# Kernel optimization log

Measured on AMD Instinct MI355X. Metric: run time of the kernel, lower is better.

Reference implementation:

```python
import jax, jax.numpy as jnp
import numpy as np

DIM = 1024
HEADS = 16
HEAD_DIM = DIM // HEADS


def setup_inputs() -> dict:
    key = jax.random.key(0)
    ks = jax.random.split(key, 10)
    B, N, M = 4, 2048, 2048
    s = 1.0 / np.sqrt(DIM)
    return {
        "x": jax.random.normal(ks[0], (B, N, DIM), jnp.float32),
        "context": jax.random.normal(ks[1], (B, M, DIM), jnp.float32),
        "Wq": jax.random.normal(ks[2], (DIM, DIM), jnp.float32) * s,
        "bq": jnp.zeros((DIM,), jnp.float32),
        "Wk": jax.random.normal(ks[3], (DIM, DIM), jnp.float32) * s,
        "bk": jnp.zeros((DIM,), jnp.float32),
        "Wv": jax.random.normal(ks[4], (DIM, DIM), jnp.float32) * s,
        "bv": jnp.zeros((DIM,), jnp.float32),
        "Wo": jax.random.normal(ks[5], (DIM, DIM), jnp.float32) * s,
        "bo": jnp.zeros((DIM,), jnp.float32),
    }


def reference(x, context, Wq, bq, Wk, bk, Wv, bv, Wo, bo):
    B, N, C = x.shape
    M = context.shape[1]
    scale = HEAD_DIM ** (-0.5)
    # projections + split heads: [B, H, L, D]
    q = (x @ Wq.T + bq).reshape(B, N, HEADS, HEAD_DIM).transpose(0, 2, 1, 3)
    k = (context @ Wk.T + bk).reshape(B, M, HEADS, HEAD_DIM).transpose(0, 2, 1, 3)
    v = (context @ Wv.T + bv).reshape(B, M, HEADS, HEAD_DIM).transpose(0, 2, 1, 3)
    attn = jax.nn.softmax(jnp.einsum('bhnd,bhmd->bhnm', q, k) * scale, axis=-1)
    out = jnp.einsum('bhnm,bhmd->bhnd', attn, v)  # [B, H, N, D]
    out = out.transpose(0, 2, 1, 3).reshape(B, N, C)
    return out @ Wo.T + bo
```

## Files before the change

### kernel.cpp

```cpp
#include <hip/hip_runtime.h>
#include <hip/hip_bf16.h>
#include <stdint.h>


#define HEADS 16
#define HD 64
#define NSEQ 2048
#define DIMSZ 1024

typedef __bf16 bf16x8_t __attribute__((ext_vector_type(8)));
typedef float f32x4_t __attribute__((ext_vector_type(4)));
typedef short s16x4 __attribute__((ext_vector_type(4)));
typedef unsigned short u16;
typedef unsigned int u32;

__device__ __forceinline__ u16 f2bf(float f) {
    union { float f; u32 i; } x; x.f = f;
    u32 r = x.i + 0x7FFF + ((x.i >> 16) & 1);
    return (u16)(r >> 16);
}
__device__ __forceinline__ u32 pk2(float a, float b) {
    __hip_bfloat162 h = __float22bfloat162_rn(float2{a, b});
    union { __hip_bfloat162 h2; u32 u; } c; c.h2 = h; return c.u;
}

#if defined(__has_builtin)
#if __has_builtin(__builtin_amdgcn_exp2f)
#define EXP2(x) __builtin_amdgcn_exp2f(x)
#endif
#endif
#ifndef EXP2
#define EXP2(x) exp2f(x)
#endif

__device__ __forceinline__ void pl32swap(u32& a, u32& b) {
    asm("v_permlane32_swap_b32 %0, %1" : "+v"(a), "+v"(b));
}
__device__ __forceinline__ void pl16swap(u32& a, u32& b) {
    asm("v_permlane16_swap_b32 %0, %1" : "+v"(a), "+v"(b));
}

#define GLDS(g, l) __builtin_amdgcn_global_load_lds( \
    (const __attribute__((address_space(1))) void*)(g), \
    (__attribute__((address_space(3))) void*)(l), 16, 0, 0)

__global__ __launch_bounds__(256)
void cvt_all(const float* __restrict__ x, const float* __restrict__ ctx,
             const float* __restrict__ wq, const float* __restrict__ wk,
             const float* __restrict__ wv, const float* __restrict__ wo,
             u16* __restrict__ xb, u16* __restrict__ ctxb,
             u16* __restrict__ wqb, u16* __restrict__ wkb,
             u16* __restrict__ wvb, u16* __restrict__ wob)
{
    long g = (long)blockIdx.x * 256 + threadIdx.x;
    const float* in; u16* out; long off;
    if (g < 1048576L)      { in = x;   out = xb;   off = g; }
    else if (g < 2097152L) { in = ctx; out = ctxb; off = g - 1048576L; }
    else if (g < 2228224L) { in = wq;  out = wqb;  off = g - 2097152L; }
    else if (g < 2359296L) { in = wk;  out = wkb;  off = g - 2228224L; }
    else if (g < 2490368L) { in = wv;  out = wvb;  off = g - 2359296L; }
    else                   { in = wo;  out = wob;  off = g - 2490368L; }
    long i = off * 8;
    float4 a = *(const float4*)(in + i);
    float4 b = *(const float4*)(in + i + 4);
    union { uint4 v; u16 h[8]; } u;
    u.h[0] = f2bf(a.x); u.h[1] = f2bf(a.y); u.h[2] = f2bf(a.z); u.h[3] = f2bf(a.w);
    u.h[4] = f2bf(b.x); u.h[5] = f2bf(b.y); u.h[6] = f2bf(b.z); u.h[7] = f2bf(b.w);
    *(uint4*)(out + i) = u.v;
}

#define BM 128
#define BN 128

#define BKQ 64

__global__ __launch_bounds__(256, 3)
void qkv_gemm(const u16* __restrict__ xb, const u16* __restrict__ ctxb,
              const u16* __restrict__ wq, const u16* __restrict__ wk,
              const u16* __restrict__ wv,
              const float* __restrict__ bq, const float* __restrict__ bk,
              const float* __restrict__ bv,
              u16* __restrict__ qo, u16* __restrict__ ko, u16* __restrict__ vo,
              float qscale)
{
    __shared__ __align__(16) u16 Asm[BM * BKQ];
    __shared__ __align__(16) u16 Wsm[BN * BKQ];

    const int g    = blockIdx.x >> 3;
    const int col0 = (blockIdx.x & 7) * BN;
    const int row0 = blockIdx.y * BM;

    const u16* A = (g == 0) ? xb : ctxb;
    const u16* W = (g == 0) ? wq : (g == 1) ? wk : wv;
    const float* bias = (g == 0) ? bq : (g == 1) ? bk : bv;
    const float scale = (g == 0) ? qscale : 1.0f;

    const int t    = threadIdx.x;
    const int lane = t & 63;
    const int wid  = t >> 6;
    const int lrow = lane & 15;
    const int lq   = lane >> 4;
    const int wm   = (wid >> 1) * 64;
    const int wn   = (wid & 1) * 64;

    const u16* gA[4]; const u16* gW[4];
    u16* lA[4]; u16* lW[4];
    #pragma unroll
    for (int q = 0; q < 4; q++) {
        int s = q * 256 + t;
        int r = s >> 3;
        int c = (s & 7) ^ (r & 7);
        gA[q] = A + (long)(row0 + r) * DIMSZ + c * 8;
        gW[q] = W + (long)(col0 + r) * DIMSZ + c * 8;
        int lofs = (q * 256 + wid * 64) * 8;
        lA[q] = &Asm[lofs];
        lW[q] = &Wsm[lofs];
    }

    f32x4_t zero = {0.f, 0.f, 0.f, 0.f};
    f32x4_t acc[4][4];
    #pragma unroll
    for (int i = 0; i < 4; i++)
        #pragma unroll
        for (int j = 0; j < 4; j++) acc[i][j] = zero;

    const int rsw = lrow & 7;

    for (int k0 = 0; k0 < DIMSZ; k0 += BKQ) {
        __syncthreads();
        #pragma unroll
        for (int q = 0; q < 4; q++) {
            GLDS(gA[q] + k0, lA[q]);
            GLDS(gW[q] + k0, lW[q]);
        }
        __syncthreads();

        #pragma unroll
        for (int kk = 0; kk < 2; kk++) {
            bf16x8_t af[4], bfr[4];
            #pragma unroll
            for (int i = 0; i < 4; i++)
                af[i] = *(const bf16x8_t*)
                    &Asm[(wm + 16 * i + lrow) * BKQ + (((kk * 4 + lq) ^ rsw) << 3)];
            #pragma unroll
            for (int j = 0; j < 4; j++)
                bfr[j] = *(const bf16x8_t*)
                    &Wsm[(wn + 16 * j + lrow) * BKQ + (((kk * 4 + lq) ^ rsw) << 3)];
            #pragma unroll
            for (int i = 0; i < 4; i++)
                #pragma unroll
                for (int j = 0; j < 4; j++)
                    acc[i][j] = __builtin_amdgcn_mfma_f32_16x16x32_bf16(
                        af[i], bfr[j], acc[i][j], 0, 0, 0);
        }
    }

    float bvv[4];
    #pragma unroll
    for (int j = 0; j < 4; j++) bvv[j] = bias[col0 + wn + 16 * j + lrow];

    if (g < 2) {
        u16* out = g ? ko : qo;
        #pragma unroll
        for (int i = 0; i < 4; i++) {
            #pragma unroll
            for (int j = 0; j < 4; j++) {
                int cc = col0 + wn + 16 * j + lrow;
                #pragma unroll
                for (int r = 0; r < 4; r++) {
                    int rr = row0 + wm + 16 * i + lq * 4 + r;
                    float v = (acc[i][j][r] + bvv[j]) * scale;
                    int b = rr >> 11, n = rr & 2047;
                    int h = cc >> 6,  d = cc & 63;
                    long oidx = ((long)((b * HEADS + h) * NSEQ + n) << 6) + d;
                    out[oidx] = f2bf(v);
                }
            }
        }
    } else {
        #pragma unroll
        for (int i = 0; i < 4; i++) {
            int n0 = row0 + wm + 16 * i + lq * 4;
            int b  = n0 >> 11, nn = n0 & 2047;
            #pragma unroll
            for (int j = 0; j < 4; j++) {
                int d = col0 + wn + 16 * j + lrow;
                uint2 p;
                p.x = pk2(acc[i][j][0] + bvv[j], acc[i][j][1] + bvv[j]);
                p.y = pk2(acc[i][j][2] + bvv[j], acc[i][j][3] + bvv[j]);
                long o = ((long)((b * HEADS + (d >> 6)) * HD + (d & 63)) << 11) + nn;
                *(uint2*)&vo[o] = p;
            }
        }
    }
}

#define BKO 64

__global__ __launch_bounds__(256, 3)
void gemm_o(const u16* __restrict__ A, const u16* __restrict__ W,
            const float* __restrict__ bias, float* __restrict__ out)
{
    __shared__ __align__(16) u16 Asm[BM * BKO];
    __shared__ __align__(16) u16 Wsm[BN * BKO];

    const int t    = threadIdx.x;
    const int lane = t & 63;
    const int wid  = t >> 6;
    const int lrow = lane & 15;
    const int lq   = lane >> 4;
    const int wm   = (wid >> 1) * 64;
    const int wn   = (wid & 1) * 64;
    const int row0 = blockIdx.y * BM;
    const int col0 = blockIdx.x * BN;

    const u16* gA[4]; const u16* gW[4];
    u16* lA[4]; u16* lW[4];
    #pragma unroll
    for (int q = 0; q < 4; q++) {
        int s = q * 256 + t;
        int r = s >> 3;
        int c = (s & 7) ^ (r & 7);
        gA[q] = A + (long)(row0 + r) * DIMSZ + c * 8;
        gW[q] = W + (long)(col0 + r) * DIMSZ + c * 8;
        int lofs = (q * 256 + wid * 64) * 8;
        lA[q] = &Asm[lofs];
        lW[q] = &Wsm[lofs];
    }

    f32x4_t zero = {0.f, 0.f, 0.f, 0.f};
    f32x4_t acc[4][4];
    #pragma unroll
    for (int i = 0; i < 4; i++)
        #pragma unroll
        for (int j = 0; j < 4; j++) acc[i][j] = zero;

    const int rsw = lrow & 7;

    for (int k0 = 0; k0 < DIMSZ; k0 += BKO) {
        __syncthreads();
        #pragma unroll
        for (int q = 0; q < 4; q++) {
            GLDS(gA[q] + k0, lA[q]);
            GLDS(gW[q] + k0, lW[q]);
        }
        __syncthreads();

        #pragma unroll
        for (int kk = 0; kk < 2; kk++) {
            bf16x8_t af[4], bfr[4];
            #pragma unroll
            for (int i = 0; i < 4; i++)
                af[i] = *(const bf16x8_t*)
                    &Asm[(wm + 16 * i + lrow) * BKO + (((kk * 4 + lq) ^ rsw) << 3)];
            #pragma unroll
            for (int j = 0; j < 4; j++)
                bfr[j] = *(const bf16x8_t*)
                    &Wsm[(wn + 16 * j + lrow) * BKO + (((kk * 4 + lq) ^ rsw) << 3)];
            #pragma unroll
            for (int i = 0; i < 4; i++)
                #pragma unroll
                for (int j = 0; j < 4; j++)
                    acc[i][j] = __builtin_amdgcn_mfma_f32_16x16x32_bf16(
                        af[i], bfr[j], acc[i][j], 0, 0, 0);
        }
    }

    float bvv[4];
    #pragma unroll
    for (int j = 0; j < 4; j++) bvv[j] = bias[col0 + wn + 16 * j + lrow];

    #pragma unroll
    for (int i = 0; i < 4; i++) {
        #pragma unroll
        for (int j = 0; j < 4; j++) {
            int cc = col0 + wn + 16 * j + lrow;
            #pragma unroll
            for (int r = 0; r < 4; r++) {
                int rr = row0 + wm + 16 * i + lq * 4 + r;
                out[(long)rr * DIMSZ + cc] = acc[i][j][r] + bvv[j];
            }
        }
    }
}

__global__ __launch_bounds__(256, 4)
void attn(const u16* __restrict__ Q, const u16* __restrict__ K,
          const u16* __restrict__ Vt, u16* __restrict__ O)
{
    __shared__ __align__(16) u16 Ksm[2][64 * 64];
    __shared__ __align__(16) u16 Vsm[2][64 * 64];

    const int t    = threadIdx.x;
    const int lane = t & 63;
    const int w    = t >> 6;
    const int lrow = lane & 15;
    const int lq   = lane >> 4;
    const int bh   = blockIdx.x;
    const int q0   = blockIdx.y * 128;
    const int b    = bh >> 4;
    const int h    = bh & 15;

    bf16x8_t qf[2][2];
    #pragma unroll
    for (int qa = 0; qa < 2; qa++) {
        const long qbase = ((long)bh * NSEQ + q0 + w * 32 + qa * 16 + lrow) * HD;
        qf[qa][0] = *(const bf16x8_t*)&Q[qbase + lq * 8];
        qf[qa][1] = *(const bf16x8_t*)&Q[qbase + lq * 8 + 32];
    }

    const long kvbase = (long)bh * NSEQ * HD;

    const u16* gK[2]; const u16* gV[2]; int lofs[2];
    #pragma unroll
    for (int c = 0; c < 2; c++) {
        int s  = c * 256 + t;
        int r  = s >> 3;
        int ch = (s & 7) ^ (r & 7);
        gK[c] = K  + kvbase + (long)r * HD + ch * 8;
        gV[c] = Vt + kvbase + (long)r * NSEQ + ch * 8;
        lofs[c] = (c * 256 + w * 64) * 8;
    }

    f32x4_t zero = {0.f, 0.f, 0.f, 0.f};
    f32x4_t oacc[2][4];
    #pragma unroll
    for (int qa = 0; qa < 2; qa++)
        #pragma unroll
        for (int jd = 0; jd < 4; jd++) oacc[qa][jd] = zero;
    f32x4_t lacc[2] = {zero, zero};

    union { u32 u[4]; bf16x8_t v; } ob;
    ob.u[0] = ob.u[1] = ob.u[2] = ob.u[3] = 0x3F803F80u;
    const bf16x8_t onesb = ob.v;

    const int rsw = lrow & 7;

    auto stage = [&](int ktn, int nb) {
        long ko = (long)ktn * (64 * HD);
        int  vo = ktn * 64;
        GLDS(gK[0] + ko, &Ksm[nb][lofs[0]]);
        GLDS(gK[1] + ko, &Ksm[nb][lofs[1]]);
        GLDS(gV[0] + vo, &Vsm[nb][lofs[0]]);
        GLDS(gV[1] + vo, &Vsm[nb][lofs[1]]);
    };

    auto tile = [&](const u16* Ks, const u16* Vs) {
        #pragma unroll
        for (int t2 = 0; t2 < 2; t2++) {
            f32x4_t sacc[2][2];
            __builtin_amdgcn_s_setprio(1);
            #pragma unroll
            for (int jh = 0; jh < 2; jh++) {
                int jt = t2 * 2 + jh;
                bf16x8_t kf0 = *(const bf16x8_t*)
                    &Ks[(16 * jt + lrow) * 64 + ((lq ^ rsw) << 3)];
                bf16x8_t kf1 = *(const bf16x8_t*)
                    &Ks[(16 * jt + lrow) * 64 + (((4 + lq) ^ rsw) << 3)];
                sacc[jh][0] = __builtin_amdgcn_mfma_f32_16x16x32_bf16(
                    kf0, qf[0][0], zero, 0, 0, 0);
                sacc[jh][1] = __builtin_amdgcn_mfma_f32_16x16x32_bf16(
                    kf0, qf[1][0], zero, 0, 0, 0);
                sacc[jh][0] = __builtin_amdgcn_mfma_f32_16x16x32_bf16(
                    kf1, qf[0][1], sacc[jh][0], 0, 0, 0);
                sacc[jh][1] = __builtin_amdgcn_mfma_f32_16x16x32_bf16(
                    kf1, qf[1][1], sacc[jh][1], 0, 0, 0);
            }
            __builtin_amdgcn_s_setprio(0);

            bf16x8_t pa32[2];
            #pragma unroll
            for (int qa = 0; qa < 2; qa++) {
                u32 uu[2][2];
                #pragma unroll
                for (int jh = 0; jh < 2; jh++) {
                    float p0 = EXP2(sacc[jh][qa][0]);
                    float p1 = EXP2(sacc[jh][qa][1]);
                    float p2 = EXP2(sacc[jh][qa][2]);
                    float p3 = EXP2(sacc[jh][qa][3]);
                    uu[jh][0] = pk2(p0, p1);
                    uu[jh][1] = pk2(p2, p3);
                }
                pl32swap(uu[0][0], uu[1][0]);
                pl16swap(uu[0][0], uu[1][0]);
                pl32swap(uu[0][1], uu[1][1]);
                pl16swap(uu[0][1], uu[1][1]);
                union { u32 u[4]; bf16x8_t v; } pk_;
                pk_.u[0] = uu[0][0]; pk_.u[1] = uu[0][1];
                pk_.u[2] = uu[1][0]; pk_.u[3] = uu[1][1];
                pa32[qa] = pk_.v;
            }

            __builtin_amdgcn_s_setprio(1);
            lacc[0] = __builtin_amdgcn_mfma_f32_16x16x32_bf16(
                pa32[0], onesb, lacc[0], 0, 0, 0);
            lacc[1] = __builtin_amdgcn_mfma_f32_16x16x32_bf16(
                pa32[1], onesb, lacc[1], 0, 0, 0);
            #pragma unroll
            for (int jd = 0; jd < 4; jd++) {
                bf16x8_t vb = *(const bf16x8_t*)
                    &Vs[(16 * jd + lrow) * 64 + (((4 * t2 + lq) ^ rsw) << 3)];
                oacc[0][jd] = __builtin_amdgcn_mfma_f32_16x16x32_bf16(
                    pa32[0], vb, oacc[0][jd], 0, 0, 0);
                oacc[1][jd] = __builtin_amdgcn_mfma_f32_16x16x32_bf16(
                    pa32[1], vb, oacc[1][jd], 0, 0, 0);
            }
            __builtin_amdgcn_s_setprio(0);
        }
    };

    stage(0, 0);
    __syncthreads();

    for (int kt = 0; kt < NSEQ / 64; kt += 2) {
        stage(kt + 1, 1);
        tile(Ksm[0], Vsm[0]);
        __syncthreads();
        if (kt + 2 < NSEQ / 64) stage(kt + 2, 0);
        tile(Ksm[1], Vsm[1]);
        __syncthreads();
    }

    float linv[2][4];
    #pragma unroll
    for (int qa = 0; qa < 2; qa++)
        #pragma unroll
        for (int r = 0; r < 4; r++)
            linv[qa][r] = __builtin_amdgcn_rcpf(lacc[qa][r]);

    #pragma unroll
    for (int qa = 0; qa < 2; qa++) {
        #pragma unroll
        for (int jd = 0; jd < 4; jd++) {
            #pragma unroll
            for (int r = 0; r < 4; r++) {
                int qrow = q0 + w * 32 + qa * 16 + lq * 4 + r;
                int d    = 16 * jd + lrow;
                long oidx = ((long)(b * NSEQ + qrow)) * DIMSZ + h * HD + d;
                O[oidx] = f2bf(oacc[qa][jd][r] * linv[qa][r]);
            }
        }
    }
}

extern "C" void kernel_launch(void* const* d_in, const int* in_sizes, int n_in,
                              void* d_out, int out_size, void* d_ws, size_t ws_size,
                              hipStream_t stream)
{
    const float* x   = (const float*)d_in[0];
    const float* ctx = (const float*)d_in[1];
    const float* Wq  = (const float*)d_in[2];
    const float* bq  = (const float*)d_in[3];
    const float* Wk  = (const float*)d_in[4];
    const float* bk  = (const float*)d_in[5];
    const float* Wv  = (const float*)d_in[6];
    const float* bv  = (const float*)d_in[7];
    const float* Wo  = (const float*)d_in[8];
    const float* bo  = (const float*)d_in[9];
    float* out = (float*)d_out;

    const size_t NX = (size_t)8192 * 1024;
    const size_t NW = (size_t)1024 * 1024;

    u16* xb   = (u16*)d_ws;
    u16* ctxb = xb + NX;
    u16* wqb  = ctxb + NX;
    u16* wkb  = wqb + NW;
    u16* wvb  = wkb + NW;
    u16* wob  = wvb + NW;
    u16* qws  = wob + NW;
    u16* kws  = qws + NX;
    u16* vws  = kws + NX;
    u16* aws  = xb;

    cvt_all<<<10240, 256, 0, stream>>>(x, ctx, Wq, Wk, Wv, Wo,
                                       xb, ctxb, wqb, wkb, wvb, wob);

    const float qscale = 0.125f * 1.44269504088896340736f;

    qkv_gemm<<<dim3(24, 8192 / BM), 256, 0, stream>>>(
        xb, ctxb, wqb, wkb, wvb, bq, bk, bv, qws, kws, vws, qscale);
    attn<<<dim3(64, NSEQ / 128), 256, 0, stream>>>(qws, kws, vws, aws);
    gemm_o<<<dim3(DIMSZ / BN, 8192 / BM), 256, 0, stream>>>(aws, wob, bo, out);
}
```

Before: 312.4 us.

## Transpose MFMA operands for vectorized Q/K/O stores and double-buffer gemm_o

For the Q/K projection and the output GEMM, the MFMA operands are swapped so each lane holds four consecutive output columns. The epilogue can then write packed bf16x4 or float4 stores with a vector bias load, instead of scattered scalar stores. gemm_o also gains a two-stage shared-memory double buffer that issues the next tile's global-to-LDS loads before computing the current one, which halves the barriers per K step. This doubles LDS use and lowers the launch-bounds occupancy hint from 3 to 2, which may reduce latency hiding.

```diff
diff --git a/kernel.cpp b/kernel.cpp
--- a/kernel.cpp
+++ b/kernel.cpp
@@ -126,58 +126,90 @@
 
     const int rsw = lrow & 7;
 
-    for (int k0 = 0; k0 < DIMSZ; k0 += BKQ) {
-        __syncthreads();
-        #pragma unroll
-        for (int q = 0; q < 4; q++) {
-            GLDS(gA[q] + k0, lA[q]);
-            GLDS(gW[q] + k0, lW[q]);
-        }
-        __syncthreads();
-
-        #pragma unroll
-        for (int kk = 0; kk < 2; kk++) {
-            bf16x8_t af[4], bfr[4];
-            #pragma unroll
-            for (int i = 0; i < 4; i++)
-                af[i] = *(const bf16x8_t*)
-                    &Asm[(wm + 16 * i + lrow) * BKQ + (((kk * 4 + lq) ^ rsw) << 3)];
-            #pragma unroll
-            for (int j = 0; j < 4; j++)
-                bfr[j] = *(const bf16x8_t*)
-                    &Wsm[(wn + 16 * j + lrow) * BKQ + (((kk * 4 + lq) ^ rsw) << 3)];
-            #pragma unroll
-            for (int i = 0; i < 4; i++)
+    if (g < 2) {
+        for (int k0 = 0; k0 < DIMSZ; k0 += BKQ) {
+            __syncthreads();
+            #pragma unroll
+            for (int q = 0; q < 4; q++) {
+                GLDS(gA[q] + k0, lA[q]);
+                GLDS(gW[q] + k0, lW[q]);
+            }
+            __syncthreads();
+
+            #pragma unroll
+            for (int kk = 0; kk < 2; kk++) {
+                bf16x8_t af[4], bfr[4];
+                #pragma unroll
+                for (int i = 0; i < 4; i++)
+                    af[i] = *(const bf16x8_t*)
+                        &Asm[(wm + 16 * i + lrow) * BKQ + (((kk * 4 + lq) ^ rsw) << 3)];
                 #pragma unroll
                 for (int j = 0; j < 4; j++)
-                    acc[i][j] = __builtin_amdgcn_mfma_f32_16x16x32_bf16(
-                        af[i], bfr[j], acc[i][j], 0, 0, 0);
-        }
-    }
-
-    float bvv[4];
-    #pragma unroll
-    for (int j = 0; j < 4; j++) bvv[j] = bias[col0 + wn + 16 * j + lrow];
-
-    if (g < 2) {
-        u16* out = g ? ko : qo;
-        #pragma unroll
-        for (int i = 0; i < 4; i++) {
-            #pragma unroll
-            for (int j = 0; j < 4; j++) {
-                int cc = col0 + wn + 16 * j + lrow;
-                #pragma unroll
-                for (int r = 0; r < 4; r++) {
-                    int rr = row0 + wm + 16 * i + lq * 4 + r;
-                    float v = (acc[i][j][r] + bvv[j]) * scale;
-                    int b = rr >> 11, n = rr & 2047;
-                    int h = cc >> 6,  d = cc & 63;
-                    long oidx = ((long)((b * HEADS + h) * NSEQ + n) << 6) + d;
-                    out[oidx] = f2bf(v);
-                }
+                    bfr[j] = *(const bf16x8_t*)
+                        &Wsm[(wn + 16 * j + lrow) * BKQ + (((kk * 4 + lq) ^ rsw) << 3)];
+                #pragma unroll
+                for (int i = 0; i < 4; i++)
+                    #pragma unroll
+                    for (int j = 0; j < 4; j++)
+                        acc[i][j] = __builtin_amdgcn_mfma_f32_16x16x32_bf16(
+                            bfr[j], af[i], acc[i][j], 0, 0, 0);
+            }
+        }
+
+        u16* outp = g ? ko : qo;
+        #pragma unroll
+        for (int j = 0; j < 4; j++) {
+            int d0 = col0 + wn + 16 * j + lq * 4;
+            f32x4_t bb = *(const f32x4_t*)&bias[d0];
+            int h  = d0 >> 6;
+            int dl = d0 & 63;
+            #pragma unroll
+            for (int i = 0; i < 4; i++) {
+                int n  = row0 + wm + 16 * i + lrow;
+                int b  = n >> 11, nn = n & 2047;
+                uint2 p;
+                p.x = pk2((acc[i][j][0] + bb[0]) * scale,
+                          (acc[i][j][1] + bb[1]) * scale);
+                p.y = pk2((acc[i][j][2] + bb[2]) * scale,
+                          (acc[i][j][3] + bb[3]) * scale);
+                long oidx = ((long)((b * HEADS + h) * NSEQ + nn) << 6) + dl;
+                *(uint2*)&outp[oidx] = p;
             }
         }
     } else {
+        for (int k0 = 0; k0 < DIMSZ; k0 += BKQ) {
+            __syncthreads();
+            #pragma unroll
+            for (int q = 0; q < 4; q++) {
+                GLDS(gA[q] + k0, lA[q]);
+                GLDS(gW[q] + k0, lW[q]);
+            }
+            __syncthreads();
+
+            #pragma unroll
+            for (int kk = 0; kk < 2; kk++) {
+                bf16x8_t af[4], bfr[4];
+                #pragma unroll
+                for (int i = 0; i < 4; i++)
+                    af[i] = *(const bf16x8_t*)
+                        &Asm[(wm + 16 * i + lrow) * BKQ + (((kk * 4 + lq) ^ rsw) << 3)];
+                #pragma unroll
+                for (int j = 0; j < 4; j++)
+                    bfr[j] = *(const bf16x8_t*)
+                        &Wsm[(wn + 16 * j + lrow) * BKQ + (((kk * 4 + lq) ^ rsw) << 3)];
+                #pragma unroll
+                for (int i = 0; i < 4; i++)
+                    #pragma unroll
+                    for (int j = 0; j < 4; j++)
+                        acc[i][j] = __builtin_amdgcn_mfma_f32_16x16x32_bf16(
+                            af[i], bfr[j], acc[i][j], 0, 0, 0);
+            }
+        }
+
+        float bvv[4];
+        #pragma unroll
+        for (int j = 0; j < 4; j++) bvv[j] = bias[col0 + wn + 16 * j + lrow];
+
         #pragma unroll
         for (int i = 0; i < 4; i++) {
             int n0 = row0 + wm + 16 * i + lq * 4;
@@ -197,12 +229,12 @@
 
 #define BKO 64
 
-__global__ __launch_bounds__(256, 3)
+__global__ __launch_bounds__(256, 2)
 void gemm_o(const u16* __restrict__ A, const u16* __restrict__ W,
             const float* __restrict__ bias, float* __restrict__ out)
 {
-    __shared__ __align__(16) u16 Asm[BM * BKO];
-    __shared__ __align__(16) u16 Wsm[BN * BKO];
+    __shared__ __align__(16) u16 Asm[2][BM * BKO];
+    __shared__ __align__(16) u16 Wsm[2][BN * BKO];
 
     const int t    = threadIdx.x;
     const int lane = t & 63;
@@ -214,8 +246,7 @@
     const int row0 = blockIdx.y * BM;
     const int col0 = blockIdx.x * BN;
 
-    const u16* gA[4]; const u16* gW[4];
-    u16* lA[4]; u16* lW[4];
+    const u16* gA[4]; const u16* gW[4]; int lofs[4];
     #pragma unroll
     for (int q = 0; q < 4; q++) {
         int s = q * 256 + t;
@@ -223,9 +254,7 @@
         int c = (s & 7) ^ (r & 7);
         gA[q] = A + (long)(row0 + r) * DIMSZ + c * 8;
         gW[q] = W + (long)(col0 + r) * DIMSZ + c * 8;
-        int lofs = (q * 256 + wid * 64) * 8;
-        lA[q] = &Asm[lofs];
-        lW[q] = &Wsm[lofs];
+        lofs[q] = (q * 256 + wid * 64) * 8;
     }
 
     f32x4_t zero = {0.f, 0.f, 0.f, 0.f};
@@ -237,49 +266,57 @@
 
     const int rsw = lrow & 7;
 
-    for (int k0 = 0; k0 < DIMSZ; k0 += BKO) {
-        __syncthreads();
+    auto stage = [&](int k0, int nb) {
         #pragma unroll
         for (int q = 0; q < 4; q++) {
-            GLDS(gA[q] + k0, lA[q]);
-            GLDS(gW[q] + k0, lW[q]);
-        }
-        __syncthreads();
-
+            GLDS(gA[q] + k0, &Asm[nb][lofs[q]]);
+            GLDS(gW[q] + k0, &Wsm[nb][lofs[q]]);
+        }
+    };
+    auto compute = [&](int nb) {
         #pragma unroll
         for (int kk = 0; kk < 2; kk++) {
             bf16x8_t af[4], bfr[4];
             #pragma unroll
             for (int i = 0; i < 4; i++)
                 af[i] = *(const bf16x8_t*)
-                    &Asm[(wm + 16 * i + lrow) * BKO + (((kk * 4 + lq) ^ rsw) << 3)];
+                    &Asm[nb][(wm + 16 * i + lrow) * BKO + (((kk * 4 + lq) ^ rsw) << 3)];
             #pragma unroll
             for (int j = 0; j < 4; j++)
                 bfr[j] = *(const bf16x8_t*)
-                    &Wsm[(wn + 16 * j + lrow) * BKO + (((kk * 4 + lq) ^ rsw) << 3)];
+                    &Wsm[nb][(wn + 16 * j + lrow) * BKO + (((kk * 4 + lq) ^ rsw) << 3)];
             #pragma unroll
             for (int i = 0; i < 4; i++)
                 #pragma unroll
                 for (int j = 0; j < 4; j++)
                     acc[i][j] = __builtin_amdgcn_mfma_f32_16x16x32_bf16(
-                        af[i], bfr[j], acc[i][j], 0, 0, 0);
-        }
-    }
-
-    float bvv[4];
-    #pragma unroll
-    for (int j = 0; j < 4; j++) bvv[j] = bias[col0 + wn + 16 * j + lrow];
-
-    #pragma unroll
-    for (int i = 0; i < 4; i++) {
-        #pragma unroll
-        for (int j = 0; j < 4; j++) {
-            int cc = col0 + wn + 16 * j + lrow;
-            #pragma unroll
-            for (int r = 0; r < 4; r++) {
-                int rr = row0 + wm + 16 * i + lq * 4 + r;
-                out[(long)rr * DIMSZ + cc] = acc[i][j][r] + bvv[j];
-            }
+                        bfr[j], af[i], acc[i][j], 0, 0, 0);
+        }
+    };
+
+    stage(0, 0);
+    __syncthreads();
+
+    for (int k0 = 0; k0 < DIMSZ; k0 += 2 * BKO) {
+        stage(k0 + BKO, 1);
+        compute(0);
+        __syncthreads();
+        if (k0 + 2 * BKO < DIMSZ) stage(k0 + 2 * BKO, 0);
+        compute(1);
+        __syncthreads();
+    }
+
+    #pragma unroll
+    for (int j = 0; j < 4; j++) {
+        int d0 = col0 + wn + 16 * j + lq * 4;
+        f32x4_t bb = *(const f32x4_t*)&bias[d0];
+        #pragma unroll
+        for (int i = 0; i < 4; i++) {
+            int n = row0 + wm + 16 * i + lrow;
+            f32x4_t v;
+            #pragma unroll
+            for (int r = 0; r < 4; r++) v[r] = acc[i][j][r] + bb[r];
+            *(f32x4_t*)&out[(long)n * DIMSZ + d0] = v;
         }
     }
 }
```

Measured after the change: 305.7 us. 2.1% less time.
